# Kernel tuning notes

Hardware: AMD Instinct MI355X
Metric: run time of the kernel (lower is better)

## Reference

```python
import math
import jax, jax.numpy as jnp
import numpy as np

HEAD_DIM = 2
ROPE_PERIOD = 19.0
OMEGA = 2.0 * math.pi / ROPE_PERIOD
PEAK_EPS = 0.3
TARGET_LOGIT_GAP = math.log(10.0)
ATTN_AMPLITUDE = TARGET_LOGIT_GAP / (math.cos(OMEGA * PEAK_EPS) - math.cos(OMEGA * (1.0 - PEAK_EPS)))
QK_NORM_SCALE = math.sqrt(ATTN_AMPLITUDE / math.sqrt(2.0))
ATTN_SCALE = HEAD_DIM ** (-0.5) * QK_NORM_SCALE ** 2
MODEL_DIM = 2
CONST_NORM = math.sqrt(MODEL_DIM)
PHI = OMEGA * (10.0 + PEAK_EPS)
VOCAB_SIZE = 10
RMS_EPS = 1e-6


def _rms_norm(x):
    return x * jax.lax.rsqrt(jnp.mean(x * x, axis=-1, keepdims=True) + RMS_EPS)


def _apply_rope(x):  # x: [B, L, 2]
    L = x.shape[1]
    theta = jnp.arange(L, dtype=x.dtype) * OMEGA
    cos_t = jnp.cos(theta)[None, :, None]
    sin_t = jnp.sin(theta)[None, :, None]
    x0, x1 = x[..., 0:1], x[..., 1:2]
    return jnp.concatenate([x0 * cos_t - x1 * sin_t, x0 * sin_t + x1 * cos_t], axis=-1)


def setup_inputs() -> dict:
    key = jax.random.key(0)
    ks = jax.random.split(key, 8)
    tokens = jax.random.randint(ks[0], (16, 2048), 0, VOCAB_SIZE)
    # 7 scalar learned params (torch inits them to zero; use small nonzero values
    # so the math — including division by C — is well-defined and grads flow)
    def p(k):
        return jax.random.uniform(k, (1,), jnp.float32, 0.5, 1.5)
    return {
        'tokens': tokens,
        'C': p(ks[1]), 'eps': p(ks[2]), 'v': p(ks[3]), 'o_scale': p(ks[4]),
        'g_base': p(ks[5]), 'g_slope': p(ks[6]), 'carry_amp': p(ks[7]),
    }


def reference(tokens, C, eps, v, o_scale, g_base, g_slope, carry_amp):
    c = C[0]
    d = jnp.arange(VOCAB_SIZE, dtype=jnp.float32)
    tab = jnp.stack([c - eps[0] * d * d, -d], axis=-1)  # [V, 2]
    h = tab[tokens]  # [B, L, 2]
    B, L, _ = h.shape
    hn = _rms_norm(h)
    cos_p, sin_p = math.cos(PHI), math.sin(PHI)
    q = jnp.stack([hn[..., 0] * cos_p, hn[..., 0] * -sin_p], axis=-1)
    k = jnp.stack([hn[..., 0], jnp.zeros_like(hn[..., 0])], axis=-1)
    vv = jnp.stack([hn[..., 1] * v[0], jnp.zeros_like(hn[..., 0])], axis=-1)
    q = _apply_rope(_rms_norm(q))
    k = _apply_rope(_rms_norm(k))
    mask = jnp.triu(jnp.full((L, L), -1e9, dtype=h.dtype), k=1)
    scores = jnp.einsum('btd,bsd->bts', q, k) * ATTN_SCALE + mask[None]
    attn = jax.nn.softmax(scores, axis=-1)
    attn_out = jnp.einsum('bts,bsd->btd', attn, vv)
    h = h + jnp.stack([jnp.zeros_like(attn_out[..., 0]), o_scale[0] * attn_out[..., 0]], axis=-1)
    hn = _rms_norm(h)
    a, gc = g_base[0], g_slope[0]
    g0 = hn[..., 0] * a + hn[..., 1] * gc
    g1 = hn[..., 0] * (a - gc / c) + hn[..., 1] * gc
    base = hn[..., 0]
    carry = carry_amp[0] * (jax.nn.relu(g1) * base - jax.nn.relu(g0) * base)
    h = h + jnp.stack([jnp.zeros_like(carry), carry], axis=-1)
    nw = jnp.stack([0.1 * c / CONST_NORM, -c / (50.0 * CONST_NORM)])
    out = _rms_norm(h) * nw
    return out @ tab.T  # [B, L, V]
```

## Files before the change

kernel.cpp:

```cpp
#include <hip/hip_runtime.h>
#include <math.h>

#ifndef M_PI
#define M_PI 3.14159265358979323846
#endif

namespace {
constexpr int kL = 2048;
constexpr int kB = 16;
constexpr int kV = 10;
constexpr int kChunk = 64;
constexpr int kBlock = 256;
constexpr int kBins  = 192;
constexpr int kBPW   = 48;
constexpr int kChunksPerSeq = kL / kChunk;
}


static __device__ __forceinline__ float rl_f(float v, int l) {
    return __uint_as_float(__builtin_amdgcn_readlane(__float_as_uint(v), (unsigned)l));
}

__global__ __launch_bounds__(kBlock)
void fused_kernel(const int* __restrict__ tokens,
                  const float* __restrict__ pC,  const float* __restrict__ pEps,
                  const float* __restrict__ pV,  const float* __restrict__ pOsc,
                  const float* __restrict__ pGb, const float* __restrict__ pGs,
                  const float* __restrict__ pCa,
                  float* __restrict__ out,
                  float A, float omega, float phi)
{
    __shared__ int   sCnt[kBins];
    __shared__ float sKc[kBins], sKs[kBins], sVv[kBins];
    __shared__ float sM[4][kChunk], sS[4][kChunk], sA[4][kChunk];

    const int tid  = threadIdx.x;
    const int w    = tid >> 6;
    const int lane = tid & 63;
    const int seq  = blockIdx.x / kChunksPerSeq;
    const int t0   = (blockIdx.x % kChunksPerSeq) * kChunk;
    const int* tok = tokens + seq * kL;

    const float c   = pC[0];
    const float eps = pEps[0];
    const float vsc = pV[0];
    const float osc = pOsc[0];
    const float ga  = pGb[0];
    const float gcs = pGs[0];
    const float cam = pCa[0];

    if (tid < kBins) {
        sCnt[tid] = 0;
        float kc = 0.f, ks = 0.f, vv = 0.f;
        if (tid < 190) {
            const int   p  = tid / 10;
            const float df = (float)(tid - p * 10);
            const float h0 = c - eps * df * df;
            const float h1 = -df;
            const float iv = rsqrtf(0.5f * (h0 * h0 + h1 * h1) + 1e-6f);
            const float n0 = h0 * iv;
            const float r  = n0 * rsqrtf(0.5f * n0 * n0 + 1e-6f);
            float sn, cs;
            __sincosf(omega * (float)p + phi, &sn, &cs);
            kc = r * cs; ks = r * sn; vv = (h1 * iv) * vsc;
        }
        sKc[tid] = kc; sKs[tid] = ks; sVv[tid] = vv;
    }
    __syncthreads();

    for (int s = tid; s < t0; s += kBlock) {
        const int d = tok[s];
        const int p = s % 19;
        atomicAdd(&sCnt[p * 10 + d], 1);
    }
    __syncthreads();

    const int blo = w * kBPW;
    const int sl  = blo + ((lane < kBPW) ? lane : 0);
    const float myKc  = sKc[sl];
    const float myKs  = sKs[sl];
    const float myVv  = sVv[sl];
    const float myCnt = (float)sCnt[sl];

    const int   t   = t0 + lane;
    const int   dt  = tok[t];
    const float dft = (float)dt;
    const float h0  = c - eps * dft * dft;
    const float h1  = -dft;
    const float ivh = rsqrtf(0.5f * (h0 * h0 + h1 * h1) + 1e-6f);
    const float hn0 = h0 * ivh;
    const float r_t = hn0 * rsqrtf(0.5f * hn0 * hn0 + 1e-6f);
    const int   pt  = t % 19;
    float snq, csq;
    __sincosf(omega * (float)pt, &snq, &csq);
    const float qc = A * r_t * csq;
    const float qs = A * r_t * snq;
    const int   mybin = pt * 10 + dt;
    const unsigned long long leInc =
        (lane == 63) ? ~0ull : ((1ull << (lane + 1)) - 1ull);

    float scArr[kBPW], cntArr[kBPW];
    float m = -INFINITY;
    #pragma unroll
    for (int i = 0; i < kBPW; ++i) {
        const unsigned long long msk = __ballot(mybin == (blo + i));
        const float cnt = rl_f(myCnt, i) + (float)__popcll(msk & leInc);
        const float sc  = fmaf(qc, rl_f(myKc, i), qs * rl_f(myKs, i));
        scArr[i]  = sc;
        cntArr[i] = cnt;
        m = fmaxf(m, (cnt > 0.f) ? sc : -INFINITY);
    }
    sM[w][lane] = m;
    __syncthreads();
    m = fmaxf(fmaxf(sM[0][lane], sM[1][lane]), fmaxf(sM[2][lane], sM[3][lane]));

    float sum = 0.f, acc = 0.f;
    #pragma unroll
    for (int i = 0; i < kBPW; ++i) {
        const float e  = (cntArr[i] > 0.f) ? __expf(scArr[i] - m) : 0.f;
        const float ce = cntArr[i] * e;
        sum += ce;
        acc = fmaf(ce, rl_f(myVv, i), acc);
    }
    sS[w][lane] = sum;
    sA[w][lane] = acc;
    __syncthreads();

    if (w == 0) {
        sum = (sS[0][lane] + sS[1][lane]) + (sS[2][lane] + sS[3][lane]);
        acc = (sA[0][lane] + sA[1][lane]) + (sA[2][lane] + sA[3][lane]);
        const float attn0 = acc / sum;

        const float h1a  = h1 + osc * attn0;
        const float inv2 = rsqrtf(0.5f * (h0 * h0 + h1a * h1a) + 1e-6f);
        const float n0   = h0 * inv2;
        const float n1   = h1a * inv2;
        const float g0   = n0 * ga + n1 * gcs;
        const float g1   = n0 * (ga - gcs / c) + n1 * gcs;
        const float carry = cam * (fmaxf(g1, 0.0f) - fmaxf(g0, 0.0f)) * n0;
        const float h1b  = h1a + carry;
        const float inv3 = rsqrtf(0.5f * (h0 * h0 + h1b * h1b) + 1e-6f);
        const float rsq2 = 0.70710678118654752f;
        const float o0   = h0  * inv3 * (0.1f * c * rsq2);
        const float o1   = h1b * inv3 * (-c * 0.02f * rsq2);

        float* op = out + (size_t)(seq * kL + t) * kV;
        #pragma unroll
        for (int j = 0; j < kV; ++j) {
            const float dj = (float)j;
            op[j] = fmaf(o0, c - eps * dj * dj, o1 * (-dj));
        }
    }
}

extern "C" void kernel_launch(void* const* d_in, const int* in_sizes, int n_in,
                              void* d_out, int out_size, void* d_ws, size_t ws_size,
                              hipStream_t stream)
{
    (void)in_sizes; (void)n_in; (void)d_ws; (void)ws_size; (void)out_size;

    const int*   tokens = (const int*)d_in[0];
    const float* C      = (const float*)d_in[1];
    const float* eps    = (const float*)d_in[2];
    const float* v      = (const float*)d_in[3];
    const float* o_sc   = (const float*)d_in[4];
    const float* g_base = (const float*)d_in[5];
    const float* g_slope= (const float*)d_in[6];
    const float* c_amp  = (const float*)d_in[7];

    const double omega = 2.0 * M_PI / 19.0;
    const double amp   = log(10.0) / (cos(omega * 0.3) - cos(omega * 0.7));
    const float  attn_scale = (float)(amp * 0.5);
    const float  phi        = (float)(omega * 10.3);

    const dim3 grid(kB * kChunksPerSeq);
    fused_kernel<<<grid, kBlock, 0, stream>>>(
        tokens, C, eps, v, o_sc, g_base, g_slope, c_amp,
        (float*)d_out, attn_scale, (float)omega, phi);
}
```

Baseline: 75.28 us.

## Double block to 8 waves, vectorize token histogram and output stores

Doubles the block to 512 threads (8 waves) so each wave scans 24 bins instead of 48, halving per-thread softmax loop length and register arrays. The prefix histogram now loads tokens as int4 in one pass (512*4 covers the full sequence) instead of a strided loop. Output logits are staged through shared memory and written as coalesced float4 stores by 160 threads rather than 10 scalar stores per lane. Adds an extra barrier and more cross-wave reduction reads, and the int4 load reads all 2048 tokens unconditionally per block.

```diff
diff --git a/kernel.cpp b/kernel.cpp
--- a/kernel.cpp
+++ b/kernel.cpp
@@ -10,9 +10,10 @@
 constexpr int kB = 16;
 constexpr int kV = 10;
 constexpr int kChunk = 64;
-constexpr int kBlock = 256;
+constexpr int kBlock = 512;
+constexpr int kWaves = 8;
 constexpr int kBins  = 192;
-constexpr int kBPW   = 48;
+constexpr int kBPW   = 24;
 constexpr int kChunksPerSeq = kL / kChunk;
 }
 
@@ -21,7 +22,7 @@
     return __uint_as_float(__builtin_amdgcn_readlane(__float_as_uint(v), (unsigned)l));
 }
 
-__global__ __launch_bounds__(kBlock)
+__global__ __launch_bounds__(kBlock, 4)
 void fused_kernel(const int* __restrict__ tokens,
                   const float* __restrict__ pC,  const float* __restrict__ pEps,
                   const float* __restrict__ pV,  const float* __restrict__ pOsc,
@@ -32,7 +33,8 @@
 {
     __shared__ int   sCnt[kBins];
     __shared__ float sKc[kBins], sKs[kBins], sVv[kBins];
-    __shared__ float sM[4][kChunk], sS[4][kChunk], sA[4][kChunk];
+    __shared__ float sM[kWaves][kChunk], sS[kWaves][kChunk], sA[kWaves][kChunk];
+    __shared__ float sO0[kChunk], sO1[kChunk];
 
     const int tid  = threadIdx.x;
     const int w    = tid >> 6;
@@ -41,6 +43,8 @@
     const int t0   = (blockIdx.x % kChunksPerSeq) * kChunk;
     const int* tok = tokens + seq * kL;
 
+    const int4 tv = *reinterpret_cast<const int4*>(tok + (tid << 2));
+    const int  dt = tok[t0 + lane];
     const float c   = pC[0];
     const float eps = pEps[0];
     const float vsc = pV[0];
@@ -68,10 +72,12 @@
     }
     __syncthreads();
 
-    for (int s = tid; s < t0; s += kBlock) {
-        const int d = tok[s];
-        const int p = s % 19;
-        atomicAdd(&sCnt[p * 10 + d], 1);
+    if ((tid << 2) < t0) {
+        const int s0 = tid << 2;
+        atomicAdd(&sCnt[(s0 % 19) * 10 + tv.x], 1);
+        atomicAdd(&sCnt[((s0 + 1) % 19) * 10 + tv.y], 1);
+        atomicAdd(&sCnt[((s0 + 2) % 19) * 10 + tv.z], 1);
+        atomicAdd(&sCnt[((s0 + 3) % 19) * 10 + tv.w], 1);
     }
     __syncthreads();
 
@@ -83,7 +89,6 @@
     const float myCnt = (float)sCnt[sl];
 
     const int   t   = t0 + lane;
-    const int   dt  = tok[t];
     const float dft = (float)dt;
     const float h0  = c - eps * dft * dft;
     const float h1  = -dft;
@@ -112,7 +117,8 @@
     }
     sM[w][lane] = m;
     __syncthreads();
-    m = fmaxf(fmaxf(sM[0][lane], sM[1][lane]), fmaxf(sM[2][lane], sM[3][lane]));
+    #pragma unroll
+    for (int j = 0; j < kWaves; ++j) m = fmaxf(m, sM[j][lane]);
 
     float sum = 0.f, acc = 0.f;
     #pragma unroll
@@ -127,8 +133,9 @@
     __syncthreads();
 
     if (w == 0) {
-        sum = (sS[0][lane] + sS[1][lane]) + (sS[2][lane] + sS[3][lane]);
-        acc = (sA[0][lane] + sA[1][lane]) + (sA[2][lane] + sA[3][lane]);
+        sum = 0.f; acc = 0.f;
+        #pragma unroll
+        for (int j = 0; j < kWaves; ++j) { sum += sS[j][lane]; acc += sA[j][lane]; }
         const float attn0 = acc / sum;
 
         const float h1a  = h1 + osc * attn0;
@@ -141,15 +148,24 @@
         const float h1b  = h1a + carry;
         const float inv3 = rsqrtf(0.5f * (h0 * h0 + h1b * h1b) + 1e-6f);
         const float rsq2 = 0.70710678118654752f;
-        const float o0   = h0  * inv3 * (0.1f * c * rsq2);
-        const float o1   = h1b * inv3 * (-c * 0.02f * rsq2);
+        sO0[lane] = h0  * inv3 * (0.1f * c * rsq2);
+        sO1[lane] = h1b * inv3 * (-c * 0.02f * rsq2);
+    }
+    __syncthreads();
 
-        float* op = out + (size_t)(seq * kL + t) * kV;
+    if (tid < (kChunk * kV) / 4) {
+        const int g = tid << 2;
+        float4 o;
+        float* po = &o.x;
         #pragma unroll
-        for (int j = 0; j < kV; ++j) {
-            const float dj = (float)j;
-            op[j] = fmaf(o0, c - eps * dj * dj, o1 * (-dj));
+        for (int k2 = 0; k2 < 4; ++k2) {
+            const int gi = g + k2;
+            const int q  = (gi * 6554) >> 16;
+            const int j  = gi - q * 10;
+            const float jf = (float)j;
+            po[k2] = fmaf(sO0[q], c - eps * jf * jf, -sO1[q] * jf);
         }
+        *reinterpret_cast<float4*>(out + (size_t)(seq * kL + t0) * kV + g) = o;
     }
 }
 
```

New measurement: 73.74 us. -2.0%, faster.
